# Kernel tuning notes

Measured on AMD Instinct MI355X. Metric: run time of the kernel, lower is better.

The kernel has to match this reference:

```python
import jax, jax.numpy as jnp
import numpy as np

B, S, D, H, DK, F = 4, 2048, 1024, 16, 64, 4096


def layer_norm(x, g, b, eps=1e-5):
    mu = jnp.mean(x, axis=-1, keepdims=True)
    var = jnp.var(x, axis=-1, keepdims=True)
    return (x - mu) * jax.lax.rsqrt(var + eps) * g + b


def setup_inputs() -> dict:
    key = jax.random.key(0)
    ks = jax.random.split(key, 16)
    s = 0.02
    return {
        "src": jax.random.normal(ks[0], (B, S, D), jnp.float32),
        # per-head q/k/v projections stacked over heads: (H, D, DK)
        "Wq": jax.random.normal(ks[1], (H, D, DK), jnp.float32) * s,
        "bq": jnp.zeros((H, DK), jnp.float32),
        "Wk": jax.random.normal(ks[2], (H, D, DK), jnp.float32) * s,
        "bk": jnp.zeros((H, DK), jnp.float32),
        "Wv": jax.random.normal(ks[3], (H, D, DK), jnp.float32) * s,
        "bv": jnp.zeros((H, DK), jnp.float32),
        "Wo": jax.random.normal(ks[4], (H * DK, D), jnp.float32) * s,
        "bo": jnp.zeros((D,), jnp.float32),
        "ln1_g": jnp.ones((D,), jnp.float32),
        "ln1_b": jnp.zeros((D,), jnp.float32),
        "W1": jax.random.normal(ks[5], (D, F), jnp.float32) * s,
        "b1": jnp.zeros((F,), jnp.float32),
        "W2": jax.random.normal(ks[6], (F, D), jnp.float32) * s,
        "b2": jnp.zeros((D,), jnp.float32),
        "ln2_g": jnp.ones((D,), jnp.float32),
        "ln2_b": jnp.zeros((D,), jnp.float32),
    }


def reference(src, Wq, bq, Wk, bk, Wv, bv, Wo, bo, ln1_g, ln1_b, W1, b1, W2, b2, ln2_g, ln2_b):
    # --- multi-head attention (all heads batched via einsum) ---
    q = jnp.einsum("bsd,hdk->bhsk", src, Wq) + bq[None, :, None, :]
    k = jnp.einsum("bsd,hdk->bhsk", src, Wk) + bk[None, :, None, :]
    v = jnp.einsum("bsd,hdk->bhsk", src, Wv) + bv[None, :, None, :]
    scale = jnp.sqrt(jnp.asarray(DK, q.dtype))
    scores = jnp.einsum("bhqk,bhsk->bhqs", q, k) / scale  # [B,H,S,S]
    p = jax.nn.softmax(scores, axis=-1)
    ctx = jnp.einsum("bhqs,bhsk->bhqk", p, v)             # [B,H,S,DK]
    ctx = ctx.transpose(0, 2, 1, 3).reshape(src.shape[0], src.shape[1], H * DK)
    attn_out = ctx @ Wo + bo
    x = layer_norm(src + attn_out, ln1_g, ln1_b)
    # --- feed-forward ---
    ff = jax.nn.relu(x @ W1 + b1) @ W2 + b2
    return layer_norm(x + ff, ln2_g, ln2_b)
```

## Files before the change

### kernel.cpp

```cpp
#include <hip/hip_runtime.h>
#include <hip/hip_bf16.h>
#include <cstddef>
#include <cstdint>

typedef __bf16 bf16;
typedef __bf16 bf16x4 __attribute__((ext_vector_type(4)));
typedef __bf16 bf16x8 __attribute__((ext_vector_type(8)));
typedef float f32x4 __attribute__((ext_vector_type(4)));
typedef float f32x16 __attribute__((ext_vector_type(16)));
typedef unsigned int u32x4 __attribute__((ext_vector_type(4)));

#define GLD_LDS16(g, l) __builtin_amdgcn_global_load_lds( \
    (const __attribute__((address_space(1))) void*)(g),   \
    (__attribute__((address_space(3))) void*)(l), 16, 0, 0)

static __device__ inline unsigned int cvtpk(float lo, float hi) {
  unsigned int r;
  asm("v_cvt_pk_bf16_f32 %0, %1, %2" : "=v"(r) : "v"(lo), "v"(hi));
  return r;
}
static __device__ inline void plswap(unsigned int& a, unsigned int& b) {
  asm("v_permlane32_swap_b32 %0, %1" : "+v"(a), "+v"(b));
}

__global__ void __launch_bounds__(256)
k_cast(const float* __restrict__ in, bf16* __restrict__ out) {
  int gid = blockIdx.x * 256 + threadIdx.x;
  f32x4 a = ((const f32x4*)in)[gid * 2];
  f32x4 b = ((const f32x4*)in)[gid * 2 + 1];
  bf16x8 o;
#pragma unroll
  for (int i = 0; i < 4; ++i) { o[i] = (bf16)a[i]; o[i + 4] = (bf16)b[i]; }
  ((bf16x8*)out)[gid] = o;
}

__global__ void __launch_bounds__(256)
k_transpose_t(const float* __restrict__ in, bf16* __restrict__ out, int R, int C) {
  __shared__ float tile[64][68];
  const int nct = C >> 6;
  const int bc = blockIdx.x % nct, br = blockIdx.x / nct;
  const int r0 = br << 6, c0 = bc << 6;
  const int t = threadIdx.x;
  const int tr = t >> 4, tc4 = (t & 15) << 2;
#pragma unroll
  for (int i = 0; i < 4; ++i)
    *(f32x4*)&tile[i * 16 + tr][tc4] =
        *(const f32x4*)&in[(size_t)(r0 + i * 16 + tr) * C + c0 + tc4];
  __syncthreads();
  const int c = t >> 2, rch = (t & 3) << 4;
  bf16 ob[16];
#pragma unroll
  for (int j = 0; j < 16; ++j) ob[j] = (bf16)tile[rch + j][c];
  bf16* dst = out + (size_t)(c0 + c) * R + r0 + rch;
  *(bf16x8*)&dst[0] = *(bf16x8*)&ob[0];
  *(bf16x8*)&dst[8] = *(bf16x8*)&ob[8];
}

__global__ void __launch_bounds__(256)
k_reorder_qkv_t(const float* __restrict__ Wq, const float* __restrict__ Wk,
                const float* __restrict__ Wv, bf16* __restrict__ WqkvT) {
  __shared__ float tile[64][68];
  const int bid = blockIdx.x;
  const int sub = bid >> 4, tl = bid & 15;
  const int proj = sub >> 4, h = sub & 15;
  const float* W = (proj == 0) ? Wq : (proj == 1) ? Wk : Wv;
  const float* src = W + (size_t)h * 65536;
  const int r0 = tl << 6;
  const int t = threadIdx.x, tr = t >> 4, tc4 = (t & 15) << 2;
#pragma unroll
  for (int i = 0; i < 4; ++i)
    *(f32x4*)&tile[i * 16 + tr][tc4] =
        *(const f32x4*)&src[(size_t)(r0 + i * 16 + tr) * 64 + tc4];
  __syncthreads();
  const int c = t >> 2, rch = (t & 3) << 4;
  bf16 ob[16];
#pragma unroll
  for (int j = 0; j < 16; ++j) ob[j] = (bf16)tile[rch + j][c];
  bf16* dst = WqkvT + ((size_t)(proj * 1024 + h * 64 + c)) * 1024 + r0 + rch;
  *(bf16x8*)&dst[0] = *(bf16x8*)&ob[0];
  *(bf16x8*)&dst[8] = *(bf16x8*)&ob[8];
}

__global__ void __launch_bounds__(256)
k_bias_qkv(const float* __restrict__ bq, const float* __restrict__ bk,
           const float* __restrict__ bv, float* __restrict__ bqkv) {
  int n = blockIdx.x * 256 + threadIdx.x;
  int proj = n >> 10, wi = n & 1023;
  const float* bb = (proj == 0) ? bq : (proj == 1) ? bk : bv;
  bqkv[n] = bb[wi];
}

template <int MODE>
__global__ void __launch_bounds__(256)
k_gemm_bt(const bf16* __restrict__ A, const bf16* __restrict__ Bt,
          const float* __restrict__ bias, void* __restrict__ outp,
          int M, int N, int K,
          bf16* __restrict__ qb, bf16* __restrict__ kb, bf16* __restrict__ vb) {
  __shared__ __align__(16) bf16 As[2][128][32];
  __shared__ __align__(16) bf16 Bs[2][128][32];
  const int tid = threadIdx.x;
  const int wave = tid >> 6, lane = tid & 63;
  const int l16 = lane & 15, lq = lane >> 4;
  const int mtiles = M >> 7;
  const int tile_m = (blockIdx.x % mtiles) << 7;
  const int tile_n = (blockIdx.x / mtiles) << 7;
  const int wm = (wave >> 1) << 6, wn = (wave & 1) << 6;

  const bf16* Arow = A + (size_t)tile_m * K;
  const bf16* Brow = Bt + (size_t)tile_n * K;
  bf16* As_f = &As[0][0][0];
  bf16* Bs_f = &Bs[0][0][0];

  int gA[4], rA[4], kA[4];
#pragma unroll
  for (int j = 0; j < 4; ++j) {
    gA[j] = j * 4 + wave;
    rA[j] = (gA[j] & 7) * 16 + (lane >> 2);
    kA[j] = (gA[j] >> 3) * 32 + (lane & 3) * 8;
  }

  f32x4 acc[4][4] = {};

  for (int k0 = 0; k0 < K; k0 += 64) {
    __syncthreads();
#pragma unroll
    for (int j = 0; j < 4; ++j) {
      GLD_LDS16(Arow + (size_t)rA[j] * K + k0 + kA[j], As_f + gA[j] * 512);
      GLD_LDS16(Brow + (size_t)rA[j] * K + k0 + kA[j], Bs_f + gA[j] * 512);
    }
    __syncthreads();
#pragma unroll
    for (int p = 0; p < 2; ++p) {
      bf16x8 af[4], bfr[4];
#pragma unroll
      for (int mi = 0; mi < 4; ++mi)
        af[mi] = *(const bf16x8*)&As[p][wm + mi * 16 + l16][lq * 8];
#pragma unroll
      for (int ni = 0; ni < 4; ++ni)
        bfr[ni] = *(const bf16x8*)&Bs[p][wn + ni * 16 + l16][lq * 8];
#pragma unroll
      for (int mi = 0; mi < 4; ++mi)
#pragma unroll
        for (int ni = 0; ni < 4; ++ni)
          acc[mi][ni] = __builtin_amdgcn_mfma_f32_16x16x32_bf16(af[mi], bfr[ni], acc[mi][ni], 0, 0, 0);
    }
  }

#pragma unroll
  for (int mi = 0; mi < 4; ++mi) {
#pragma unroll
    for (int ni = 0; ni < 4; ++ni) {
      const int gn = tile_n + wn + ni * 16 + l16;
      const float bb = bias[gn];
      f32x4 v = acc[mi][ni];
      const int gm0 = tile_m + wm + mi * 16 + lq * 4;
      if (MODE == 0) {
        int proj = gn >> 10, wi = gn & 1023;
        int h = wi >> 6, dk = wi & 63;
        int b = gm0 >> 11, sdx = gm0 & 2047;
        size_t bhs = (size_t)((b << 4) + h);
        if (proj == 0) {
#pragma unroll
          for (int i = 0; i < 4; ++i)
            qb[(bhs * 2048 + sdx + i) * 64 + dk] = (bf16)((v[i] + bb) * 0.18033688f);
        } else if (proj == 1) {
#pragma unroll
          for (int i = 0; i < 4; ++i)
            kb[(bhs * 2048 + sdx + i) * 64 + dk] = (bf16)(v[i] + bb);
        } else {
          bf16x4 pk;
#pragma unroll
          for (int i = 0; i < 4; ++i) pk[i] = (bf16)(v[i] + bb);
          *(bf16x4*)&vb[(bhs * 64 + dk) * 2048 + sdx] = pk;
        }
      } else if (MODE == 1) {
#pragma unroll
        for (int i = 0; i < 4; ++i)
          ((bf16*)outp)[(size_t)(gm0 + i) * N + gn] = (bf16)(v[i] + bb);
      } else {
#pragma unroll
        for (int i = 0; i < 4; ++i)
          ((bf16*)outp)[(size_t)(gm0 + i) * N + gn] = (bf16)fmaxf(v[i] + bb, 0.f);
      }
    }
  }
}

__global__ void __launch_bounds__(256, 2)
k_attn(const bf16* __restrict__ qb, const bf16* __restrict__ kb,
       const bf16* __restrict__ vb, bf16* __restrict__ ctx) {
  __shared__ __align__(16) bf16 KsL[2][4096];
  __shared__ __align__(16) bf16 VsL[2][4096];

  const int bid = blockIdx.x;
  const int wg = (bid & 7) * 64 + (bid >> 3);
  const int bh = wg >> 3, qt = wg & 7;

  const bf16* Qp  = qb + (size_t)bh * 131072 + (size_t)qt * 16384;
  const bf16* Kbh = kb + (size_t)bh * 131072;
  const bf16* Vbh = vb + (size_t)bh * 131072;

  const int tid = threadIdx.x, wave = tid >> 6, lane = tid & 63;
  const int l31 = lane & 31, hi = lane >> 5;

  bf16x8 qfA[4], qfB[4];
  {
    const bf16* qra = Qp + (size_t)(wave * 64 + l31) * 64 + hi * 8;
    const bf16* qrb = qra + 32 * 64;
#pragma unroll
    for (int kd = 0; kd < 4; ++kd) {
      qfA[kd] = *(const bf16x8*)(qra + kd * 16);
      qfB[kd] = *(const bf16x8*)(qrb + kd * 16);
    }
  }

  const int c0 = tid, c1 = tid + 256;
  const int sw0 = ((c0 ^ (c0 >> 3)) & 7) * 8, rw0 = c0 >> 3;
  const int sw1 = ((c1 ^ (c1 >> 3)) & 7) * 8, rw1 = c1 >> 3;
  const int kof0 = rw0 * 64 + sw0, kof1 = rw1 * 64 + sw1;
  const int vof0 = rw0 * 2048 + sw0, vof1 = rw1 * 2048 + sw1;

  const int xr = (hi << 4) ^ ((l31 & 7) << 4);
  const int rb = l31 * 128 + xr;

  f32x16 oA[2] = {}, oB[2] = {};
  float lA = 0.f, lB = 0.f;

#define STAGE_KV(buf, s0)                                             \
  do {                                                                \
    GLD_LDS16(Kbh + (size_t)(s0) * 64 + kof0, &KsL[buf][c0 * 8]);     \
    GLD_LDS16(Kbh + (size_t)(s0) * 64 + kof1, &KsL[buf][c1 * 8]);     \
    GLD_LDS16(Vbh + (s0) + vof0, &VsL[buf][c0 * 8]);                  \
    GLD_LDS16(Vbh + (s0) + vof1, &VsL[buf][c1 * 8]);                  \
  } while (0)

  STAGE_KV(0, 0);
  __syncthreads();

  for (int kt = 0; kt < 32; ++kt) {
    const int cur = kt & 1;
    if (kt < 31) STAGE_KV(cur ^ 1, (kt + 1) * 64);

    const char* Kc = (const char*)&KsL[cur][0];
    const char* Vc = (const char*)&VsL[cur][0];

    bf16x8 paA[4], paB[4];
#pragma unroll
    for (int st = 0; st < 2; ++st) {
      f32x16 sA = {}, sB = {};
      __builtin_amdgcn_s_setprio(1);
#pragma unroll
      for (int kd = 0; kd < 4; ++kd) {
        bf16x8 a = *(const bf16x8*)(Kc + st * 4096 + (rb ^ (kd << 5)));
        sA = __builtin_amdgcn_mfma_f32_32x32x16_bf16(a, qfA[kd], sA, 0, 0, 0);
        sB = __builtin_amdgcn_mfma_f32_32x32x16_bf16(a, qfB[kd], sB, 0, 0, 0);
      }
      __builtin_amdgcn_s_setprio(0);

      float eA[16], eB[16];
#pragma unroll
      for (int i = 0; i < 16; ++i) {
        eA[i] = exp2f(sA[i]); lA += eA[i];
        eB[i] = exp2f(sB[i]); lB += eB[i];
      }
      unsigned int qdA[4][2], qdB[4][2];
#pragma unroll
      for (int g = 0; g < 4; ++g)
#pragma unroll
        for (int w = 0; w < 2; ++w) {
          qdA[g][w] = cvtpk(eA[g * 4 + w * 2], eA[g * 4 + w * 2 + 1]);
          qdB[g][w] = cvtpk(eB[g * 4 + w * 2], eB[g * 4 + w * 2 + 1]);
        }
#pragma unroll
      for (int a2 = 0; a2 < 2; ++a2) {
        unsigned int x0 = qdA[2 * a2][0], y0 = qdA[2 * a2 + 1][0];
        unsigned int x1 = qdA[2 * a2][1], y1 = qdA[2 * a2 + 1][1];
        plswap(x0, y0); plswap(x1, y1);
        u32x4 fA = {x0, x1, y0, y1};
        paA[st * 2 + a2] = __builtin_bit_cast(bf16x8, fA);
        unsigned int u0 = qdB[2 * a2][0], v0 = qdB[2 * a2 + 1][0];
        unsigned int u1 = qdB[2 * a2][1], v1 = qdB[2 * a2 + 1][1];
        plswap(u0, v0); plswap(u1, v1);
        u32x4 fB = {u0, u1, v0, v1};
        paB[st * 2 + a2] = __builtin_bit_cast(bf16x8, fB);
      }
    }

    __builtin_amdgcn_s_setprio(1);
#pragma unroll
    for (int nd = 0; nd < 2; ++nd)
#pragma unroll
      for (int ks = 0; ks < 4; ++ks) {
        bf16x8 vf = *(const bf16x8*)(Vc + nd * 4096 + (rb ^ (ks << 5)));
        oA[nd] = __builtin_amdgcn_mfma_f32_32x32x16_bf16(paA[ks], vf, oA[nd], 0, 0, 0);
        oB[nd] = __builtin_amdgcn_mfma_f32_32x32x16_bf16(paB[ks], vf, oB[nd], 0, 0, 0);
      }
    __builtin_amdgcn_s_setprio(0);

    __syncthreads();
  }
#undef STAGE_KV

  const float ltA = lA + __shfl_xor(lA, 32);
  const float ltB = lB + __shfl_xor(lB, 32);
  const float ivA = 1.f / ltA;
  const float ivB = 1.f / ltB;

  const int b = bh >> 4, h = bh & 15;
  const size_t rowbase = (size_t)(b * 2048 + qt * 256 + wave * 64);
#pragma unroll
  for (int r = 0; r < 16; ++r) {
    const int qr = (r & 3) + 8 * (r >> 2) + 4 * hi;
    const float dA = __shfl(ivA, qr);
    const float dB = __shfl(ivB, qr);
#pragma unroll
    for (int nd = 0; nd < 2; ++nd) {
      const int dk = nd * 32 + l31;
      ctx[(rowbase + qr) * 1024 + h * 64 + dk]      = (bf16)(oA[nd][r] * dA);
      ctx[(rowbase + 32 + qr) * 1024 + h * 64 + dk] = (bf16)(oB[nd][r] * dB);
    }
  }
}

template <typename RT, typename DT, typename OT>
__global__ void __launch_bounds__(256)
k_ln(const RT* __restrict__ resid, const DT* __restrict__ delta,
     const float* __restrict__ g, const float* __restrict__ bta,
     OT* __restrict__ out) {
  const int row = blockIdx.x, tid = threadIdx.x;
  const int wave = tid >> 6, lane = tid & 63;
  __shared__ float rs_[4], rs2_[4];
  const RT* r = resid + (size_t)row * 1024;
  const DT* d = delta + (size_t)row * 1024;
  OT* o = out + (size_t)row * 1024;
  float x[4], s = 0.f, s2 = 0.f;
#pragma unroll
  for (int j = 0; j < 4; ++j) {
    int idx = tid + j * 256;
    float v = (float)r[idx] + (float)d[idx];
    x[j] = v; s += v; s2 += v * v;
  }
#pragma unroll
  for (int m = 32; m >= 1; m >>= 1) { s += __shfl_xor(s, m); s2 += __shfl_xor(s2, m); }
  if (lane == 0) { rs_[wave] = s; rs2_[wave] = s2; }
  __syncthreads();
  float ts = rs_[0] + rs_[1] + rs_[2] + rs_[3];
  float ts2 = rs2_[0] + rs2_[1] + rs2_[2] + rs2_[3];
  float mean = ts * (1.f / 1024.f);
  float var = ts2 * (1.f / 1024.f) - mean * mean;
  float rstd = rsqrtf(var + 1e-5f);
#pragma unroll
  for (int j = 0; j < 4; ++j) {
    int idx = tid + j * 256;
    o[idx] = (OT)((x[j] - mean) * rstd * g[idx] + bta[idx]);
  }
}

extern "C" void kernel_launch(void* const* d_in, const int* in_sizes, int n_in,
                              void* d_out, int out_size, void* d_ws, size_t ws_size,
                              hipStream_t stream) {
  const float* src  = (const float*)d_in[0];
  const float* Wq   = (const float*)d_in[1];
  const float* bq   = (const float*)d_in[2];
  const float* Wk   = (const float*)d_in[3];
  const float* bk   = (const float*)d_in[4];
  const float* Wv   = (const float*)d_in[5];
  const float* bv   = (const float*)d_in[6];
  const float* Wo   = (const float*)d_in[7];
  const float* bo   = (const float*)d_in[8];
  const float* ln1g = (const float*)d_in[9];
  const float* ln1b = (const float*)d_in[10];
  const float* W1   = (const float*)d_in[11];
  const float* b1   = (const float*)d_in[12];
  const float* W2   = (const float*)d_in[13];
  const float* b2   = (const float*)d_in[14];
  const float* ln2g = (const float*)d_in[15];
  const float* ln2b = (const float*)d_in[16];

  char* p = (char*)d_ws;
  bf16*  WqkvT = (bf16*)p;  p += (size_t)3072 * 1024 * 2;
  float* bqkv  = (float*)p; p += 16384;
  bf16*  WoT   = (bf16*)p;  p += (size_t)1024 * 1024 * 2;
  bf16*  W1T   = (bf16*)p;  p += (size_t)4096 * 1024 * 2;
  bf16*  W2T   = (bf16*)p;  p += (size_t)1024 * 4096 * 2;
  bf16*  srcb  = (bf16*)p;  p += (size_t)8388608 * 2;
  bf16*  qbuf  = (bf16*)p;  p += (size_t)8388608 * 2;
  bf16*  kbuf  = (bf16*)p;  p += (size_t)8388608 * 2;
  bf16*  vbuf  = (bf16*)p;  p += (size_t)8388608 * 2;
  bf16*  ctx   = (bf16*)p;  p += (size_t)8388608 * 2;
  bf16*  x1    = (bf16*)p;  p += (size_t)8388608 * 2;
  bf16*  ff1   = (bf16*)p;  p += (size_t)8192 * 4096 * 2;
  bf16*  tmp   = qbuf;

  k_cast<<<4096, 256, 0, stream>>>(src, srcb);
  k_reorder_qkv_t<<<768, 256, 0, stream>>>(Wq, Wk, Wv, WqkvT);
  k_bias_qkv<<<12, 256, 0, stream>>>(bq, bk, bv, bqkv);
  k_transpose_t<<<256, 256, 0, stream>>>(Wo, WoT, 1024, 1024);
  k_transpose_t<<<1024, 256, 0, stream>>>(W1, W1T, 1024, 4096);
  k_transpose_t<<<1024, 256, 0, stream>>>(W2, W2T, 4096, 1024);

  k_gemm_bt<0><<<64 * 24, 256, 0, stream>>>(srcb, WqkvT, bqkv, nullptr,
                                            8192, 3072, 1024, qbuf, kbuf, vbuf);
  k_attn<<<512, 256, 0, stream>>>(qbuf, kbuf, vbuf, ctx);
  k_gemm_bt<1><<<64 * 8, 256, 0, stream>>>(ctx, WoT, bo, tmp,
                                           8192, 1024, 1024, nullptr, nullptr, nullptr);
  k_ln<float, bf16, bf16><<<8192, 256, 0, stream>>>(src, tmp, ln1g, ln1b, x1);
  k_gemm_bt<2><<<64 * 32, 256, 0, stream>>>(x1, W1T, b1, ff1,
                                            8192, 4096, 1024, nullptr, nullptr, nullptr);
  k_gemm_bt<1><<<64 * 8, 256, 0, stream>>>(ff1, W2T, b2, tmp,
                                           8192, 1024, 4096, nullptr, nullptr, nullptr);
  k_ln<bf16, bf16, float><<<8192, 256, 0, stream>>>(x1, tmp, ln2g, ln2b, (float*)d_out);
}
```

Before: 526.9 us.

## Triple-buffer attention K/V staging with vmcnt waits and raw exp2

Switches the attention kernel's K/V LDS staging from double to triple buffering. It prefetches two tiles ahead and uses an explicit vmcnt wait plus a single barrier per iteration instead of two __syncthreads. It also replaces exp2f with the hardware v_exp_f32 intrinsic and sums the row denominators as a tree instead of serially. The aim is to hide global-load latency and shorten the softmax ALU chain, at the cost of 50% more LDS, which may reduce occupancy, and a slightly different accuracy for exp2 of very negative inputs.

After: 513.9 us. 2.5% less time.

```diff
diff --git a/kernel.cpp b/kernel.cpp
--- a/kernel.cpp
+++ b/kernel.cpp
@@ -21,6 +21,18 @@
 }
 static __device__ inline void plswap(unsigned int& a, unsigned int& b) {
   asm("v_permlane32_swap_b32 %0, %1" : "+v"(a), "+v"(b));
+}
+static __device__ inline float fexp2(float x) {
+#if __has_builtin(__builtin_amdgcn_exp2f)
+  return __builtin_amdgcn_exp2f(x);
+#else
+  float r; asm("v_exp_f32 %0, %1" : "=v"(r) : "v"(x)); return r;
+#endif
+}
+static __device__ inline float tsum16(const float* e) {
+  float s0 = e[0] + e[1], s1 = e[2] + e[3], s2 = e[4] + e[5], s3 = e[6] + e[7];
+  float s4 = e[8] + e[9], s5 = e[10] + e[11], s6 = e[12] + e[13], s7 = e[14] + e[15];
+  return ((s0 + s1) + (s2 + s3)) + ((s4 + s5) + (s6 + s7));
 }
 
 __global__ void __launch_bounds__(256)
@@ -189,8 +201,8 @@
 __global__ void __launch_bounds__(256, 2)
 k_attn(const bf16* __restrict__ qb, const bf16* __restrict__ kb,
        const bf16* __restrict__ vb, bf16* __restrict__ ctx) {
-  __shared__ __align__(16) bf16 KsL[2][4096];
-  __shared__ __align__(16) bf16 VsL[2][4096];
+  __shared__ __align__(16) bf16 KsL[3][4096];
+  __shared__ __align__(16) bf16 VsL[3][4096];
 
   const int bid = blockIdx.x;
   const int wg = (bid & 7) * 64 + (bid >> 3);
@@ -235,11 +247,20 @@
   } while (0)
 
   STAGE_KV(0, 0);
-  __syncthreads();
-
+  STAGE_KV(1, 64);
+
+  int cur = 0;
   for (int kt = 0; kt < 32; ++kt) {
-    const int cur = kt & 1;
-    if (kt < 31) STAGE_KV(cur ^ 1, (kt + 1) * 64);
+    __builtin_amdgcn_sched_barrier(0);
+    if (kt == 31) { asm volatile("s_waitcnt vmcnt(0)" ::: "memory"); }
+    else          { asm volatile("s_waitcnt vmcnt(4)" ::: "memory"); }
+    __builtin_amdgcn_s_barrier();
+    __builtin_amdgcn_sched_barrier(0);
+
+    if (kt < 30) {
+      int nx = cur + 2; if (nx >= 3) nx -= 3;
+      STAGE_KV(nx, (kt + 2) * 64);
+    }
 
     const char* Kc = (const char*)&KsL[cur][0];
     const char* Vc = (const char*)&VsL[cur][0];
@@ -260,9 +281,11 @@
       float eA[16], eB[16];
 #pragma unroll
       for (int i = 0; i < 16; ++i) {
-        eA[i] = exp2f(sA[i]); lA += eA[i];
-        eB[i] = exp2f(sB[i]); lB += eB[i];
+        eA[i] = fexp2(sA[i]);
+        eB[i] = fexp2(sB[i]);
       }
+      lA += tsum16(eA);
+      lB += tsum16(eB);
       unsigned int qdA[4][2], qdB[4][2];
 #pragma unroll
       for (int g = 0; g < 4; ++g)
@@ -297,7 +320,7 @@
       }
     __builtin_amdgcn_s_setprio(0);
 
-    __syncthreads();
+    if (++cur == 3) cur = 0;
   }
 #undef STAGE_KV
 
```
